# Kernel tuning notes

Measured on AMD Instinct MI355X. Metric: run time of the kernel, lower is better.

## Reference

```python
import jax, jax.numpy as jnp
import numpy as np

N = 50000      # nodes
E = 800000     # edges (avg degree 16)
D = 128        # in_channels
H = 128        # hidden_channels


def sage_conv(x, edge_index, W_l, b_l, W_r):
    """PyG SAGEConv with aggr='mean': lin_l(mean_j x_j) + lin_r(x_i).
    edge_index[0] = source (j), edge_index[1] = destination (i)."""
    src, dst = edge_index[0], edge_index[1]
    n = x.shape[0]
    msg = x[src]                                               # [E, D] gather
    agg = jax.ops.segment_sum(msg, dst, num_segments=n)        # [N, D] scatter-sum
    cnt = jax.ops.segment_sum(jnp.ones((src.shape[0],), x.dtype), dst, num_segments=n)
    agg = agg / jnp.maximum(cnt, 1.0)[:, None]                 # mean (0 for isolated nodes)
    return agg @ W_l.T + b_l + x @ W_r.T


def setup_inputs() -> dict:
    key = jax.random.key(0)
    ks = jax.random.split(key, 9)
    s_in = 1.0 / np.sqrt(D)
    s_h = 1.0 / np.sqrt(H)
    return {
        "x": jax.random.normal(ks[0], (N, D), dtype=jnp.float32),
        "edge_index": jax.random.randint(ks[1], (2, E), 0, N, dtype=jnp.int64),
        "W1l": jax.random.uniform(ks[2], (H, D), jnp.float32, -s_in, s_in),
        "b1l": jnp.zeros((H,), jnp.float32),
        "W1r": jax.random.uniform(ks[3], (H, D), jnp.float32, -s_in, s_in),
        "W2l": jax.random.uniform(ks[4], (H, H), jnp.float32, -s_h, s_h),
        "b2l": jnp.zeros((H,), jnp.float32),
        "W2r": jax.random.uniform(ks[5], (H, H), jnp.float32, -s_h, s_h),
        "W3l": jax.random.uniform(ks[6], (H, H), jnp.float32, -s_h, s_h),
        "b3l": jnp.zeros((H,), jnp.float32),
        "W3r": jax.random.uniform(ks[7], (H, H), jnp.float32, -s_h, s_h),
    }


def reference(x, edge_index, W1l, b1l, W1r, W2l, b2l, W2r, W3l, b3l, W3r):
    x1 = sage_conv(x, edge_index, W1l, b1l, W1r)
    x1 = jax.nn.relu(x1)  # Dropout(0.5) treated as identity (eval mode)
    h_ = sage_conv(x1, edge_index, W2l, b2l, W2r)
    h = sage_conv(x1, edge_index, W3l, b3l, W3r)
    return (h_, h)
```

## Files before the change

kernel.cpp:

```cpp
#include <hip/hip_runtime.h>
#include <stdint.h>
#include <math.h>

typedef __attribute__((ext_vector_type(8))) short short8;
typedef __attribute__((ext_vector_type(4))) float float4v;
typedef __attribute__((ext_vector_type(4))) unsigned int uint4v;

__device__ __forceinline__ uint16_t f2bf(float f){
  union { float f; uint32_t i; } c; c.f = f;
  uint32_t r = c.i + 0x7fffu + ((c.i >> 16) & 1u);
  return (uint16_t)(r >> 16);
}
__device__ __forceinline__ uint32_t pack2(float lo, float hi){
  return (uint32_t)f2bf(lo) | ((uint32_t)f2bf(hi) << 16);
}
__device__ __forceinline__ void acc_bf2(uint32_t w, float& x, float& y){
  union { uint32_t i; float f; } a, b;
  a.i = w << 16; b.i = w & 0xffff0000u;
  x += a.f; y += b.f;
}
__device__ __forceinline__ void accum8(uint4 v, float* a){
  acc_bf2(v.x, a[0], a[1]); acc_bf2(v.y, a[2], a[3]);
  acc_bf2(v.z, a[4], a[5]); acc_bf2(v.w, a[6], a[7]);
}



#define P1_EPT 8

__global__ __launch_bounds__(512) void prep_kernel(
    const int* __restrict__ ei, int E, int NB, int CAP,
    int* __restrict__ fill, int2* __restrict__ bins, int p1blk,
    const float* __restrict__ x,
    const float* __restrict__ w0, const float* __restrict__ w1,
    const float* __restrict__ w2, const float* __restrict__ w3,
    const float* __restrict__ w4, const float* __restrict__ w5,
    uint16_t* __restrict__ xb, uint16_t* __restrict__ wb, int nx){
  if ((int)blockIdx.x < p1blk){
    __shared__ int hist[256], base[256], cur[256];
    int tid = threadIdx.x;
    if (tid < 256){ hist[tid] = 0; cur[tid] = 0; }
    __syncthreads();
    int src[P1_EPT], dst[P1_EPT];
    int e0 = blockIdx.x * (512 * P1_EPT);
    #pragma unroll
    for (int k = 0; k < P1_EPT; ++k){
      int e = e0 + k * 512 + tid;
      bool ok = e < E;
      src[k] = ok ? ei[e] : 0;
      dst[k] = ok ? ei[E + e] : -1;
      if (ok) atomicAdd(&hist[dst[k] >> 8], 1);
    }
    __syncthreads();
    if (tid < NB && hist[tid] > 0) base[tid] = atomicAdd(&fill[tid], hist[tid]);
    __syncthreads();
    #pragma unroll
    for (int k = 0; k < P1_EPT; ++k){
      if (dst[k] >= 0){
        int b = dst[k] >> 8;
        int loc = base[b] + atomicAdd(&cur[b], 1);
        if (loc < CAP) bins[(size_t)b * CAP + loc] = make_int2(src[k], dst[k]);
      }
    }
  } else {
    int i = (blockIdx.x - p1blk) * 512 + threadIdx.x;
    int stride = (gridDim.x - p1blk) * 512;
    int nnode = nx >> 7;
    for (int j = i; j < (nx >> 2); j += stride){
      float4 v = ((const float4*)x)[j];
      int node = j >> 5;
      int col = (j & 31) * 4;
      uint2 o;
      o.x = pack2(v.x, v.y); o.y = pack2(v.z, v.w);
      *(uint2*)(xb + ((size_t)(col >> 5) * nnode + node) * 32 + (col & 31)) = o;
    }
    const int WSZ = 128 * 128;
    for (int j = i; j < 6 * WSZ; j += stride){
      int t = j >> 14, o = j & (WSZ - 1);
      const float* w = t == 0 ? w0 : t == 1 ? w1 : t == 2 ? w2 : t == 3 ? w3 : t == 4 ? w4 : w5;
      wb[j] = f2bf(w[o]);
    }
  }
}


__global__ __launch_bounds__(512) void build_kernel(const int2* __restrict__ bins,
                                                    const int* __restrict__ fill,
                                                    int CAP, int n,
                                                    int2* __restrict__ rowptr2,
                                                    int* __restrict__ esrc){
  __shared__ int h[256], s[256], cursor[256];
  int b = blockIdx.x, tid = threadIdx.x;
  int cnt = fill[b]; if (cnt > CAP) cnt = CAP;
  int gbase = b * CAP;
  if (tid < 256) h[tid] = 0;
  __syncthreads();
  for (int i = tid; i < cnt; i += 512)
    atomicAdd(&h[bins[(size_t)gbase + i].y & 255], 1);
  __syncthreads();
  if (tid < 256) s[tid] = h[tid];
  __syncthreads();
  #pragma unroll
  for (int off = 1; off < 256; off <<= 1){
    int v = 0;
    if (tid < 256 && tid >= off) v = s[tid - off];
    __syncthreads();
    if (tid < 256) s[tid] += v;
    __syncthreads();
  }
  if (tid < 256){
    int node = (b << 8) + tid;
    int excl = s[tid] - h[tid];
    if (node < n) rowptr2[node] = make_int2(gbase + excl, gbase + s[tid]);
    cursor[tid] = gbase + excl;
  }
  __syncthreads();
  for (int i = tid; i < cnt; i += 512){
    int2 e = bins[(size_t)gbase + i];
    int p = atomicAdd(&cursor[e.y & 255], 1);
    esrc[p] = e.x;
  }
}


__global__ __launch_bounds__(256) void agg_kernel(const uint16_t* __restrict__ xin,
                                                  const int2* __restrict__ rowptr2,
                                                  const int* __restrict__ esrc,
                                                  uint16_t* __restrict__ aggw, int n){
  int b = blockIdx.x;
  int x8 = b & 7;
  int pass = x8 >> 1;
  int chunk = (b >> 3) * 2 + (x8 & 1);
  int wid = threadIdx.x >> 6, lane = threadIdx.x & 63;
  int g = lane >> 2, fq = lane & 3;
  int node = chunk * 64 + wid * 16 + g;
  bool valid = node < n;
  int ni = valid ? node : 0;
  int2 be = rowptr2[ni];
  int beg = be.x, end = valid ? be.y : be.x;
  float inv = 1.f / fmaxf((float)(end - beg), 1.f);
  const uint4* xv = (const uint4*)(xin + (size_t)pass * n * 32);
  float a[8] = {0.f,0.f,0.f,0.f,0.f,0.f,0.f,0.f};
  int e = beg;
  for (; e + 3 < end; e += 4){
    int s0 = __builtin_nontemporal_load(esrc + e);
    int s1 = __builtin_nontemporal_load(esrc + e + 1);
    int s2 = __builtin_nontemporal_load(esrc + e + 2);
    int s3 = __builtin_nontemporal_load(esrc + e + 3);
    uint4 v0 = xv[(size_t)s0 * 4 + fq];
    uint4 v1 = xv[(size_t)s1 * 4 + fq];
    uint4 v2 = xv[(size_t)s2 * 4 + fq];
    uint4 v3 = xv[(size_t)s3 * 4 + fq];
    accum8(v0, a); accum8(v1, a); accum8(v2, a); accum8(v3, a);
  }
  for (; e < end; ++e){
    int s = __builtin_nontemporal_load(esrc + e);
    uint4 v = xv[(size_t)s * 4 + fq];
    accum8(v, a);
  }
  if (valid){
    uint4v o;
    o.x = pack2(a[0] * inv, a[1] * inv);
    o.y = pack2(a[2] * inv, a[3] * inv);
    o.z = pack2(a[4] * inv, a[5] * inv);
    o.w = pack2(a[6] * inv, a[7] * inv);
    __builtin_nontemporal_store(o,
        (uint4v*)(aggw + (size_t)pass * n * 32) + (size_t)node * 4 + fq);
  }
}


#define WT_STRIDE 136

__device__ __forceinline__ void stage_weights(const uint16_t* __restrict__ Wl,
                                              const uint16_t* __restrict__ Wr,
                                              int ch, uint16_t* lds_l,
                                              uint16_t* lds_r, int tid){
  const uint4* srcL = (const uint4*)(Wl + (size_t)(ch * 64) * 128);
  const uint4* srcR = (const uint4*)(Wr + (size_t)(ch * 64) * 128);
  #pragma unroll
  for (int i = 0; i < 4; ++i){
    int j = tid + i * 256;
    int row = j >> 4, c8 = j & 15;
    uint4 vl = srcL[j], vr = srcR[j];
    *(uint4*)(lds_l + row * WT_STRIDE + c8 * 8) = vl;
    *(uint4*)(lds_r + row * WT_STRIDE + c8 * 8) = vr;
  }
}

__global__ __launch_bounds__(256) void gemm1_kernel(
    const uint16_t* __restrict__ Aagg, const uint16_t* __restrict__ Ax,
    const uint16_t* __restrict__ Wl, const uint16_t* __restrict__ Wr,
    const float* __restrict__ bias, uint16_t* __restrict__ x1b, int n){
  __shared__ uint16_t lds_l[64 * WT_STRIDE], lds_r[64 * WT_STRIDE];
  int tid = threadIdx.x, lane = tid & 63, wid = tid >> 6;
  int m = lane & 15, quad = lane >> 4;
  int ch = blockIdx.y;
  int r0 = blockIdx.x * 64 + wid * 16;
  int arow = r0 + m; if (arow > n - 1) arow = n - 1;

  short8 a0f[4], a1f[4];
  #pragma unroll
  for (int ks = 0; ks < 4; ++ks){
    a0f[ks] = *(const short8*)(Aagg + ((size_t)ks * n + arow) * 32 + quad * 8);
    a1f[ks] = *(const short8*)(Ax   + ((size_t)ks * n + arow) * 32 + quad * 8);
  }
  stage_weights(Wl, Wr, ch, lds_l, lds_r, tid);
  __syncthreads();

  float4v acc[4];
  #pragma unroll
  for (int ct = 0; ct < 4; ++ct) acc[ct] = (float4v){0.f, 0.f, 0.f, 0.f};
  #pragma unroll
  for (int ks = 0; ks < 4; ++ks){
    #pragma unroll
    for (int ct = 0; ct < 4; ++ct){
      short8 b0 = *(const short8*)(lds_l + (ct * 16 + m) * WT_STRIDE + ks * 32 + quad * 8);
      acc[ct] = __builtin_amdgcn_mfma_f32_16x16x32_bf16(a0f[ks], b0, acc[ct], 0, 0, 0);
      short8 b1 = *(const short8*)(lds_r + (ct * 16 + m) * WT_STRIDE + ks * 32 + quad * 8);
      acc[ct] = __builtin_amdgcn_mfma_f32_16x16x32_bf16(a1f[ks], b1, acc[ct], 0, 0, 0);
    }
  }
  #pragma unroll
  for (int ct = 0; ct < 4; ++ct){
    int col = ch * 64 + ct * 16 + m;
    float bv = bias[col];
    size_t base = ((size_t)(col >> 5) * n) * 32 + (col & 31);
    #pragma unroll
    for (int i = 0; i < 4; ++i){
      int grow = r0 + quad * 4 + i;
      if (grow < n)
        x1b[base + (size_t)grow * 32] = f2bf(fmaxf(acc[ct][i] + bv, 0.f));
    }
  }
}

__global__ __launch_bounds__(256) void gemm23_kernel(
    const uint16_t* __restrict__ Aagg, const uint16_t* __restrict__ Ax,
    const uint16_t* __restrict__ W2l, const uint16_t* __restrict__ W2r,
    const float* __restrict__ b2,
    const uint16_t* __restrict__ W3l, const uint16_t* __restrict__ W3r,
    const float* __restrict__ b3,
    float* __restrict__ out, size_t half, int n){
  __shared__ uint16_t lds_l[64 * WT_STRIDE], lds_r[64 * WT_STRIDE];
  int tid = threadIdx.x, lane = tid & 63, wid = tid >> 6;
  int m = lane & 15, quad = lane >> 4;
  int ch = blockIdx.y & 1, pass = blockIdx.y >> 1;
  const uint16_t* Wl = pass ? W3l : W2l;
  const uint16_t* Wr = pass ? W3r : W2r;
  const float*    bb = pass ? b3  : b2;
  float* op = out + (pass ? half : 0);
  int r0 = blockIdx.x * 64 + wid * 16;
  int arow = r0 + m; if (arow > n - 1) arow = n - 1;

  short8 a0f[4], a1f[4];
  #pragma unroll
  for (int ks = 0; ks < 4; ++ks){
    a0f[ks] = *(const short8*)(Aagg + ((size_t)ks * n + arow) * 32 + quad * 8);
    a1f[ks] = *(const short8*)(Ax   + ((size_t)ks * n + arow) * 32 + quad * 8);
  }
  stage_weights(Wl, Wr, ch, lds_l, lds_r, tid);
  __syncthreads();

  float4v acc[4];
  #pragma unroll
  for (int ct = 0; ct < 4; ++ct) acc[ct] = (float4v){0.f, 0.f, 0.f, 0.f};
  #pragma unroll
  for (int ks = 0; ks < 4; ++ks){
    #pragma unroll
    for (int ct = 0; ct < 4; ++ct){
      short8 b0 = *(const short8*)(lds_l + (ct * 16 + m) * WT_STRIDE + ks * 32 + quad * 8);
      acc[ct] = __builtin_amdgcn_mfma_f32_16x16x32_bf16(a0f[ks], b0, acc[ct], 0, 0, 0);
      short8 b1 = *(const short8*)(lds_r + (ct * 16 + m) * WT_STRIDE + ks * 32 + quad * 8);
      acc[ct] = __builtin_amdgcn_mfma_f32_16x16x32_bf16(a1f[ks], b1, acc[ct], 0, 0, 0);
    }
  }
  #pragma unroll
  for (int ct = 0; ct < 4; ++ct){
    int col = ch * 64 + ct * 16 + m;
    float bv = bb[col];
    #pragma unroll
    for (int i = 0; i < 4; ++i){
      int grow = r0 + quad * 4 + i;
      if (grow < n) op[(size_t)grow * 128 + col] = acc[ct][i] + bv;
    }
  }
}


extern "C" void kernel_launch(void* const* d_in, const int* in_sizes, int n_in,
                              void* d_out, int out_size, void* d_ws, size_t ws_size,
                              hipStream_t stream) {
  const float* x   = (const float*)d_in[0];
  const int*   ei  = (const int*)d_in[1];
  const float* W1l = (const float*)d_in[2];
  const float* b1l = (const float*)d_in[3];
  const float* W1r = (const float*)d_in[4];
  const float* W2l = (const float*)d_in[5];
  const float* b2l = (const float*)d_in[6];
  const float* W2r = (const float*)d_in[7];
  const float* W3l = (const float*)d_in[8];
  const float* b3l = (const float*)d_in[9];
  const float* W3r = (const float*)d_in[10];
  float* out = (float*)d_out;

  const int n = in_sizes[0] / 128;
  const int E = in_sizes[1] / 2;
  const size_t half = (size_t)n * 128;
  const int WSZ = 128 * 128;

  const int NB = (n + 255) >> 8;
  int mean = (E + NB - 1) / NB;
  int CAP = mean + 8 * (int)sqrt((double)mean) + 64;
  CAP = (CAP + 63) & ~63;

  size_t off = 0;
  auto carve = [&](size_t bytes) -> void* {
    void* p = (char*)d_ws + off;
    off += (bytes + 255) & ~(size_t)255;
    return p;
  };
  int2*     rowptr2 = (int2*)carve((size_t)n * 8);
  int*      fill    = (int*)carve((size_t)NB * 4);
  int*      esrc    = (int*)carve((size_t)NB * CAP * 4);
  uint16_t* xb      = (uint16_t*)carve(half * 2);
  uint16_t* wb      = (uint16_t*)carve((size_t)6 * WSZ * 2);
  uint16_t* x1b     = (uint16_t*)carve(half * 2);
  uint16_t* agg     = (uint16_t*)carve(half * 2);
  int2*     bins    = (int2*)carve((size_t)NB * CAP * 8);
  (void)ws_size;

  hipMemsetAsync(fill, 0, (size_t)NB * 4, stream);

  int p1blk = (E + 512 * P1_EPT - 1) / (512 * P1_EPT);
  int cblk  = 256;
  prep_kernel<<<p1blk + cblk, 512, 0, stream>>>(ei, E, NB, CAP, fill, bins, p1blk,
                                                x, W1l, W1r, W2l, W2r, W3l, W3r,
                                                xb, wb, (int)half);
  build_kernel<<<NB, 512, 0, stream>>>(bins, fill, CAP, n, rowptr2, esrc);

  int chunks = (n + 63) / 64;
  int npairs = (chunks + 1) / 2;
  int agrid = npairs * 8;
  int gblk = (n + 63) / 64;
  const uint16_t *Wb1l = wb, *Wb1r = wb + WSZ, *Wb2l = wb + 2 * WSZ,
                 *Wb2r = wb + 3 * WSZ, *Wb3l = wb + 4 * WSZ, *Wb3r = wb + 5 * WSZ;

  agg_kernel<<<agrid, 256, 0, stream>>>(xb, rowptr2, esrc, agg, n);
  gemm1_kernel<<<dim3(gblk, 2), 256, 0, stream>>>(agg, xb, Wb1l, Wb1r, b1l, x1b, n);

  agg_kernel<<<agrid, 256, 0, stream>>>(x1b, rowptr2, esrc, agg, n);
  gemm23_kernel<<<dim3(gblk, 4), 256, 0, stream>>>(agg, x1b, Wb2l, Wb2r, b2l,
                                                   Wb3l, Wb3r, b3l, out, half, n);
}
```

Measured before the change: 240.8 us.

## Narrow feature slabs to 16 columns and loop weight chunks inside GEMM blocks

Feature storage changes from 4 slabs of 32 bf16 columns to 8 slabs of 16 columns. Each aggregation thread pair now covers one node's 16-column slab, giving 8 column passes with 128 nodes per block. The GEMM kernels now load the A fragments once per block and loop over the output-column chunks (and both layers for the second GEMM), restaging weights in LDS each time. This removes the repeated A-fragment global reads across blockIdx.y, at the cost of fewer, serialized blocks with extra barriers.

New measurement: 275.5 us. 1.14x slower.

```diff
diff --git a/kernel.cpp b/kernel.cpp
--- a/kernel.cpp
+++ b/kernel.cpp
@@ -72,7 +72,7 @@
       int col = (j & 31) * 4;
       uint2 o;
       o.x = pack2(v.x, v.y); o.y = pack2(v.z, v.w);
-      *(uint2*)(xb + ((size_t)(col >> 5) * nnode + node) * 32 + (col & 31)) = o;
+      *(uint2*)(xb + ((size_t)(col >> 4) * nnode + node) * 16 + (col & 15)) = o;
     }
     const int WSZ = 128 * 128;
     for (int j = i; j < 6 * WSZ; j += stride){
@@ -128,18 +128,16 @@
                                                   const int* __restrict__ esrc,
                                                   uint16_t* __restrict__ aggw, int n){
   int b = blockIdx.x;
-  int x8 = b & 7;
-  int pass = x8 >> 1;
-  int chunk = (b >> 3) * 2 + (x8 & 1);
+  int pass = b & 7;
+  int chunk = b >> 3;
   int wid = threadIdx.x >> 6, lane = threadIdx.x & 63;
-  int g = lane >> 2, fq = lane & 3;
-  int node = chunk * 64 + wid * 16 + g;
+  int g = lane >> 1, h = lane & 1;
+  int node = chunk * 128 + wid * 32 + g;
   bool valid = node < n;
-  int ni = valid ? node : 0;
-  int2 be = rowptr2[ni];
+  int2 be = rowptr2[valid ? node : 0];
   int beg = be.x, end = valid ? be.y : be.x;
   float inv = 1.f / fmaxf((float)(end - beg), 1.f);
-  const uint4* xv = (const uint4*)(xin + (size_t)pass * n * 32);
+  const uint4* xv = (const uint4*)(xin + (size_t)pass * n * 16);
   float a[8] = {0.f,0.f,0.f,0.f,0.f,0.f,0.f,0.f};
   int e = beg;
   for (; e + 3 < end; e += 4){
@@ -147,15 +145,15 @@
     int s1 = __builtin_nontemporal_load(esrc + e + 1);
     int s2 = __builtin_nontemporal_load(esrc + e + 2);
     int s3 = __builtin_nontemporal_load(esrc + e + 3);
-    uint4 v0 = xv[(size_t)s0 * 4 + fq];
-    uint4 v1 = xv[(size_t)s1 * 4 + fq];
-    uint4 v2 = xv[(size_t)s2 * 4 + fq];
-    uint4 v3 = xv[(size_t)s3 * 4 + fq];
+    uint4 v0 = xv[(size_t)s0 * 2 + h];
+    uint4 v1 = xv[(size_t)s1 * 2 + h];
+    uint4 v2 = xv[(size_t)s2 * 2 + h];
+    uint4 v3 = xv[(size_t)s3 * 2 + h];
     accum8(v0, a); accum8(v1, a); accum8(v2, a); accum8(v3, a);
   }
   for (; e < end; ++e){
     int s = __builtin_nontemporal_load(esrc + e);
-    uint4 v = xv[(size_t)s * 4 + fq];
+    uint4 v = xv[(size_t)s * 2 + h];
     accum8(v, a);
   }
   if (valid){
@@ -165,7 +163,7 @@
     o.z = pack2(a[4] * inv, a[5] * inv);
     o.w = pack2(a[6] * inv, a[7] * inv);
     __builtin_nontemporal_store(o,
-        (uint4v*)(aggw + (size_t)pass * n * 32) + (size_t)node * 4 + fq);
+        (uint4v*)(aggw + (size_t)pass * n * 16) + (size_t)node * 2 + h);
   }
 }
 
@@ -188,6 +186,18 @@
   }
 }
 
+__device__ __forceinline__ void load_afrag(const uint16_t* __restrict__ Aagg,
+                                           const uint16_t* __restrict__ Ax,
+                                           int arow, int quad, int n,
+                                           short8* a0f, short8* a1f){
+  #pragma unroll
+  for (int ks = 0; ks < 4; ++ks){
+    int slab = 2 * ks + (quad >> 1), off = (quad & 1) * 8;
+    a0f[ks] = *(const short8*)(Aagg + ((size_t)slab * n + arow) * 16 + off);
+    a1f[ks] = *(const short8*)(Ax   + ((size_t)slab * n + arow) * 16 + off);
+  }
+}
+
 __global__ __launch_bounds__(256) void gemm1_kernel(
     const uint16_t* __restrict__ Aagg, const uint16_t* __restrict__ Ax,
     const uint16_t* __restrict__ Wl, const uint16_t* __restrict__ Wr,
@@ -195,42 +205,40 @@
   __shared__ uint16_t lds_l[64 * WT_STRIDE], lds_r[64 * WT_STRIDE];
   int tid = threadIdx.x, lane = tid & 63, wid = tid >> 6;
   int m = lane & 15, quad = lane >> 4;
-  int ch = blockIdx.y;
   int r0 = blockIdx.x * 64 + wid * 16;
   int arow = r0 + m; if (arow > n - 1) arow = n - 1;
 
   short8 a0f[4], a1f[4];
-  #pragma unroll
-  for (int ks = 0; ks < 4; ++ks){
-    a0f[ks] = *(const short8*)(Aagg + ((size_t)ks * n + arow) * 32 + quad * 8);
-    a1f[ks] = *(const short8*)(Ax   + ((size_t)ks * n + arow) * 32 + quad * 8);
-  }
-  stage_weights(Wl, Wr, ch, lds_l, lds_r, tid);
-  __syncthreads();
-
-  float4v acc[4];
-  #pragma unroll
-  for (int ct = 0; ct < 4; ++ct) acc[ct] = (float4v){0.f, 0.f, 0.f, 0.f};
-  #pragma unroll
-  for (int ks = 0; ks < 4; ++ks){
+  load_afrag(Aagg, Ax, arow, quad, n, a0f, a1f);
+
+  for (int ch = 0; ch < 2; ++ch){
+    if (ch) __syncthreads();
+    stage_weights(Wl, Wr, ch, lds_l, lds_r, tid);
+    __syncthreads();
+    float4v acc[4];
+    #pragma unroll
+    for (int ct = 0; ct < 4; ++ct) acc[ct] = (float4v){0.f, 0.f, 0.f, 0.f};
+    #pragma unroll
+    for (int ks = 0; ks < 4; ++ks){
+      #pragma unroll
+      for (int ct = 0; ct < 4; ++ct){
+        short8 b0 = *(const short8*)(lds_l + (ct * 16 + m) * WT_STRIDE + ks * 32 + quad * 8);
+        acc[ct] = __builtin_amdgcn_mfma_f32_16x16x32_bf16(a0f[ks], b0, acc[ct], 0, 0, 0);
+        short8 b1 = *(const short8*)(lds_r + (ct * 16 + m) * WT_STRIDE + ks * 32 + quad * 8);
+        acc[ct] = __builtin_amdgcn_mfma_f32_16x16x32_bf16(a1f[ks], b1, acc[ct], 0, 0, 0);
+      }
+    }
     #pragma unroll
     for (int ct = 0; ct < 4; ++ct){
-      short8 b0 = *(const short8*)(lds_l + (ct * 16 + m) * WT_STRIDE + ks * 32 + quad * 8);
-      acc[ct] = __builtin_amdgcn_mfma_f32_16x16x32_bf16(a0f[ks], b0, acc[ct], 0, 0, 0);
-      short8 b1 = *(const short8*)(lds_r + (ct * 16 + m) * WT_STRIDE + ks * 32 + quad * 8);
-      acc[ct] = __builtin_amdgcn_mfma_f32_16x16x32_bf16(a1f[ks], b1, acc[ct], 0, 0, 0);
-    }
-  }
-  #pragma unroll
-  for (int ct = 0; ct < 4; ++ct){
-    int col = ch * 64 + ct * 16 + m;
-    float bv = bias[col];
-    size_t base = ((size_t)(col >> 5) * n) * 32 + (col & 31);
-    #pragma unroll
-    for (int i = 0; i < 4; ++i){
-      int grow = r0 + quad * 4 + i;
-      if (grow < n)
-        x1b[base + (size_t)grow * 32] = f2bf(fmaxf(acc[ct][i] + bv, 0.f));
+      int col = ch * 64 + ct * 16 + m;
+      float bv = bias[col];
+      size_t base = (size_t)(ch * 4 + ct) * n * 16 + m;
+      #pragma unroll
+      for (int i = 0; i < 4; ++i){
+        int grow = r0 + quad * 4 + i;
+        if (grow < n)
+          x1b[base + (size_t)grow * 16] = f2bf(fmaxf(acc[ct][i] + bv, 0.f));
+      }
     }
   }
 }
@@ -245,44 +253,43 @@
   __shared__ uint16_t lds_l[64 * WT_STRIDE], lds_r[64 * WT_STRIDE];
   int tid = threadIdx.x, lane = tid & 63, wid = tid >> 6;
   int m = lane & 15, quad = lane >> 4;
-  int ch = blockIdx.y & 1, pass = blockIdx.y >> 1;
-  const uint16_t* Wl = pass ? W3l : W2l;
-  const uint16_t* Wr = pass ? W3r : W2r;
-  const float*    bb = pass ? b3  : b2;
-  float* op = out + (pass ? half : 0);
   int r0 = blockIdx.x * 64 + wid * 16;
   int arow = r0 + m; if (arow > n - 1) arow = n - 1;
 
   short8 a0f[4], a1f[4];
-  #pragma unroll
-  for (int ks = 0; ks < 4; ++ks){
-    a0f[ks] = *(const short8*)(Aagg + ((size_t)ks * n + arow) * 32 + quad * 8);
-    a1f[ks] = *(const short8*)(Ax   + ((size_t)ks * n + arow) * 32 + quad * 8);
-  }
-  stage_weights(Wl, Wr, ch, lds_l, lds_r, tid);
-  __syncthreads();
-
-  float4v acc[4];
-  #pragma unroll
-  for (int ct = 0; ct < 4; ++ct) acc[ct] = (float4v){0.f, 0.f, 0.f, 0.f};
-  #pragma unroll
-  for (int ks = 0; ks < 4; ++ks){
+  load_afrag(Aagg, Ax, arow, quad, n, a0f, a1f);
+
+  for (int idx = 0; idx < 4; ++idx){
+    int pass = idx >> 1, ch = idx & 1;
+    const uint16_t* Wl = pass ? W3l : W2l;
+    const uint16_t* Wr = pass ? W3r : W2r;
+    if (idx) __syncthreads();
+    stage_weights(Wl, Wr, ch, lds_l, lds_r, tid);
+    __syncthreads();
+    float4v acc[4];
+    #pragma unroll
+    for (int ct = 0; ct < 4; ++ct) acc[ct] = (float4v){0.f, 0.f, 0.f, 0.f};
+    #pragma unroll
+    for (int ks = 0; ks < 4; ++ks){
+      #pragma unroll
+      for (int ct = 0; ct < 4; ++ct){
+        short8 b0 = *(const short8*)(lds_l + (ct * 16 + m) * WT_STRIDE + ks * 32 + quad * 8);
+        acc[ct] = __builtin_amdgcn_mfma_f32_16x16x32_bf16(a0f[ks], b0, acc[ct], 0, 0, 0);
+        short8 b1 = *(const short8*)(lds_r + (ct * 16 + m) * WT_STRIDE + ks * 32 + quad * 8);
+        acc[ct] = __builtin_amdgcn_mfma_f32_16x16x32_bf16(a1f[ks], b1, acc[ct], 0, 0, 0);
+      }
+    }
+    const float* bb = pass ? b3 : b2;
+    float* op = out + (pass ? half : 0);
     #pragma unroll
     for (int ct = 0; ct < 4; ++ct){
-      short8 b0 = *(const short8*)(lds_l + (ct * 16 + m) * WT_STRIDE + ks * 32 + quad * 8);
-      acc[ct] = __builtin_amdgcn_mfma_f32_16x16x32_bf16(a0f[ks], b0, acc[ct], 0, 0, 0);
-      short8 b1 = *(const short8*)(lds_r + (ct * 16 + m) * WT_STRIDE + ks * 32 + quad * 8);
-      acc[ct] = __builtin_amdgcn_mfma_f32_16x16x32_bf16(a1f[ks], b1, acc[ct], 0, 0, 0);
-    }
-  }
-  #pragma unroll
-  for (int ct = 0; ct < 4; ++ct){
-    int col = ch * 64 + ct * 16 + m;
-    float bv = bb[col];
-    #pragma unroll
-    for (int i = 0; i < 4; ++i){
-      int grow = r0 + quad * 4 + i;
-      if (grow < n) op[(size_t)grow * 128 + col] = acc[ct][i] + bv;
+      int col = ch * 64 + ct * 16 + m;
+      float bv = bb[col];
+      #pragma unroll
+      for (int i = 0; i < 4; ++i){
+        int grow = r0 + quad * 4 + i;
+        if (grow < n) op[(size_t)grow * 128 + col] = acc[ct][i] + bv;
+      }
     }
   }
 }
@@ -339,17 +346,16 @@
                                                 xb, wb, (int)half);
   build_kernel<<<NB, 512, 0, stream>>>(bins, fill, CAP, n, rowptr2, esrc);
 
-  int chunks = (n + 63) / 64;
-  int npairs = (chunks + 1) / 2;
-  int agrid = npairs * 8;
+  int chunks = (n + 127) / 128;
+  int agrid = chunks * 8;
   int gblk = (n + 63) / 64;
   const uint16_t *Wb1l = wb, *Wb1r = wb + WSZ, *Wb2l = wb + 2 * WSZ,
                  *Wb2r = wb + 3 * WSZ, *Wb3l = wb + 4 * WSZ, *Wb3r = wb + 5 * WSZ;
 
   agg_kernel<<<agrid, 256, 0, stream>>>(xb, rowptr2, esrc, agg, n);
-  gemm1_kernel<<<dim3(gblk, 2), 256, 0, stream>>>(agg, xb, Wb1l, Wb1r, b1l, x1b, n);
+  gemm1_kernel<<<gblk, 256, 0, stream>>>(agg, xb, Wb1l, Wb1r, b1l, x1b, n);
 
   agg_kernel<<<agrid, 256, 0, stream>>>(x1b, rowptr2, esrc, agg, n);
-  gemm23_kernel<<<dim3(gblk, 4), 256, 0, stream>>>(agg, x1b, Wb2l, Wb2r, b2l,
-                                                   Wb3l, Wb3r, b3l, out, half, n);
-}
+  gemm23_kernel<<<gblk, 256, 0, stream>>>(agg, x1b, Wb2l, Wb2r, b2l,
+                                          Wb3l, Wb3r, b3l, out, half, n);
+}
```
